# Kernel tuning notes

Measured on AMD Instinct MI355X. Metric: run time of the kernel, lower is better.

The kernel has to match this reference:

```python
import jax, jax.numpy as jnp
import numpy as np

D = 768        # d_model
F = 8192       # dict_size
N_UP = 3       # number of upstream autoencoders
K = 64         # topk
B, S = 2, 1024


def setup_inputs() -> dict:
    key = jax.random.key(0)
    ks = jax.random.split(key, 10)
    sc = 1.0 / np.sqrt(D)
    return {
        "feature_buffer": jnp.zeros((B, S, F), jnp.float32),
        "x": jax.random.normal(ks[0], (B, S, D), jnp.float32),
        "up_feats": jax.random.uniform(ks[1], (N_UP, B, S, F), jnp.float32),
        "W_enc": jax.random.normal(ks[2], (D, F), jnp.float32) * sc,
        "b_enc": jax.random.normal(ks[3], (F,), jnp.float32) * 0.01,
        "W_dec": jax.random.normal(ks[4], (F, D), jnp.float32) * sc,
        "b_dec": jax.random.normal(ks[5], (D,), jnp.float32) * 0.01,
        "up_W_dec": jax.random.normal(ks[6], (N_UP, F, D), jnp.float32) * sc,
        "up_b_dec": jax.random.normal(ks[7], (N_UP, D), jnp.float32) * 0.01,
        "conn_mask": jax.random.randint(ks[8], (N_UP, F, F), 0, 2).astype(bool),
        "k": K,
    }


def reference(feature_buffer, x, up_feats, W_enc, b_enc, W_dec, b_dec,
              up_W_dec, up_b_dec, conn_mask, k):
    # initial contribs: residual stream through current encoder
    approx = jnp.einsum("bsd,df->bsf", x, W_enc)            # [B,S,F]
    upstream_bias = jnp.zeros((D,), x.dtype)
    # accumulate pruned contributions from each upstream AE
    for i in range(up_feats.shape[0]):
        upstream_bias = upstream_bias + up_b_dec[i]
        # virtual weights up_dict -> down_dict, pruned by connection mask
        virt = (up_W_dec[i] @ W_enc) * conn_mask[i].astype(x.dtype)  # [F_up,F_down]
        approx = approx + jnp.einsum("bsf,fg->bsg", up_feats[i], virt)
    # bias correction: upstream decoder biases through encoder, plus encoder bias
    approx = approx + upstream_bias @ W_enc + b_enc          # [B,S,F]
    # topk + relu + scatter into the feature buffer
    top_vals, top_idx = jax.lax.top_k(approx, k)             # [B,S,k]
    top_vals = jax.nn.relu(top_vals)
    flat = feature_buffer.reshape(-1, F)
    rows = jnp.arange(flat.shape[0])[:, None]
    feat = flat.at[rows, top_idx.reshape(-1, k)].set(top_vals.reshape(-1, k))
    feat = feat.reshape(feature_buffer.shape)
    # decode
    return jnp.einsum("bsf,fd->bsd", feat, W_dec) + b_dec
```

## Files before the change

### kernel.cpp

```cpp
#include <hip/hip_runtime.h>
#include <hip/hip_bf16.h>


#define D_DIM 768
#define F_DIM 8192

typedef _Float16 f16;
typedef _Float16 f16x8 __attribute__((ext_vector_type(8)));
typedef float f32x4 __attribute__((ext_vector_type(4)));

#define BMN 128
#define BKK 64
#define LDSPLANE 16384

__device__ inline void split_f32(float v, f16& h, f16& l) {
    float hf = (float)(f16)v;
    if (__builtin_fabsf(hf) < 6.1035156e-5f) hf = 0.f;
    h = (f16)hf;
    l = (f16)((v - hf) * 2048.0f);
}

template<int MODE>
__global__ __launch_bounds__(256, 2)
void mfma_gemm(const f16* __restrict__ Ahp, const f16* __restrict__ Alp, int lda,
               const f16* __restrict__ Bhp, const f16* __restrict__ Blp, int ldb,
               float* __restrict__ C, int ldc,
               f16* __restrict__ Vh, f16* __restrict__ Vl,
               const float* __restrict__ bias,
               const unsigned char* __restrict__ conn, int upIdx,
               const int* __restrict__ flagp,
               int K, int fdBase)
{
    __shared__ char lds[65536];
    const int tid = threadIdx.x;
    const int bm = blockIdx.y * BMN;
    const int bn = blockIdx.x * BMN;
    const int w  = tid >> 6;
    const int l  = tid & 63;
    const int wr = (w >> 1) * 64;
    const int wc = (w & 1) * 64;

    const char* gsrc[16];
    #pragma unroll
    for (int j = 0; j < 16; ++j) {
        const int c = tid + 256 * j;
        const int p = c >> 10;
        const int q = c & 1023;
        const int r = q >> 3;
        const int sp = q & 7;
        const int slog = sp ^ (r & 7);
        const f16* base; int ld; int row0;
        if (p == 0)      { base = Ahp; ld = lda; row0 = bm; }
        else if (p == 1) { base = Alp; ld = lda; row0 = bm; }
        else if (p == 2) { base = Bhp; ld = ldb; row0 = bn; }
        else             { base = Blp; ld = ldb; row0 = bn; }
        gsrc[j] = (const char*)(base + (size_t)(row0 + r) * ld) + slog * 16;
    }

    f32x4 accH[4][4], accM[4][4];
    const f32x4 zero = {0.f, 0.f, 0.f, 0.f};
    #pragma unroll
    for (int a = 0; a < 4; ++a)
        #pragma unroll
        for (int b = 0; b < 4; ++b) { accH[a][b] = zero; accM[a][b] = zero; }

    const int steps = K >> 6;
    for (int t = 0; t < steps; ++t) {
        __syncthreads();
        #pragma unroll
        for (int j = 0; j < 16; ++j) {
            __builtin_amdgcn_global_load_lds(
                (const __attribute__((address_space(1))) void*)gsrc[j],
                (__attribute__((address_space(3))) void*)(lds + (tid + 256 * j) * 16),
                16, 0, 0);
            gsrc[j] += 128;
        }
        __syncthreads();

        #pragma unroll
        for (int kb = 0; kb < 2; ++kb) {
            const int slot = kb * 4 + (l >> 4);
            const int fr = l & 15;
            f16x8 ah[4], bh[4];
            #pragma unroll
            for (int mf = 0; mf < 4; ++mf) {
                const int r = wr + mf * 16 + fr;
                ah[mf] = *(const f16x8*)(lds + 0 * LDSPLANE + r * 128 + (slot ^ (r & 7)) * 16);
            }
            #pragma unroll
            for (int nf = 0; nf < 4; ++nf) {
                const int r = wc + nf * 16 + fr;
                bh[nf] = *(const f16x8*)(lds + 2 * LDSPLANE + r * 128 + (slot ^ (r & 7)) * 16);
            }
            #pragma unroll
            for (int nf = 0; nf < 4; ++nf)
                #pragma unroll
                for (int mf = 0; mf < 4; ++mf)
                    accH[mf][nf] = __builtin_amdgcn_mfma_f32_16x16x32_f16(
                        ah[mf], bh[nf], accH[mf][nf], 0, 0, 0);
            #pragma unroll
            for (int nf = 0; nf < 4; ++nf) {
                const int r = wc + nf * 16 + fr;
                const f16x8 bl = *(const f16x8*)(lds + 3 * LDSPLANE + r * 128 + (slot ^ (r & 7)) * 16);
                #pragma unroll
                for (int mf = 0; mf < 4; ++mf)
                    accM[mf][nf] = __builtin_amdgcn_mfma_f32_16x16x32_f16(
                        ah[mf], bl, accM[mf][nf], 0, 0, 0);
            }
            #pragma unroll
            for (int mf = 0; mf < 4; ++mf) {
                const int r = wr + mf * 16 + fr;
                const f16x8 al = *(const f16x8*)(lds + 1 * LDSPLANE + r * 128 + (slot ^ (r & 7)) * 16);
                #pragma unroll
                for (int nf = 0; nf < 4; ++nf)
                    accM[mf][nf] = __builtin_amdgcn_mfma_f32_16x16x32_f16(
                        al, bh[nf], accM[mf][nf], 0, 0, 0);
            }
        }
    }

    const float MS = 4.8828125e-4f;
    const int flag = (MODE == 1) ? *flagp : 0;

    #pragma unroll
    for (int mf = 0; mf < 4; ++mf) {
        const int row0 = wr + mf * 16 + (l >> 4) * 4;
        #pragma unroll
        for (int nf = 0; nf < 4; ++nf) {
            const int col = wc + nf * 16 + (l & 15);
            float v[4];
            #pragma unroll
            for (int rr = 0; rr < 4; ++rr)
                v[rr] = accH[mf][nf][rr] + accM[mf][nf][rr] * MS;

            if (MODE == 0) {
                const float bb = bias[bn + col];
                #pragma unroll
                for (int rr = 0; rr < 4; ++rr)
                    C[(size_t)(bm + row0 + rr) * ldc + (bn + col)] = v[rr] + bb;
            } else if (MODE == 2) {
                #pragma unroll
                for (int rr = 0; rr < 4; ++rr) {
                    float* cp = &C[(size_t)(bm + row0 + rr) * ldc + (bn + col)];
                    *cp = *cp + v[rr];
                }
            } else {
                const size_t fu = (size_t)(bn + col);
                const size_t fd0 = (size_t)(fdBase + bm + row0);
                int m[4];
                if (flag == 1) {
                    const int4 mm = *(const int4*)((const int*)conn +
                        (size_t)upIdx * F_DIM * F_DIM + fu * F_DIM + fd0);
                    m[0] = mm.x; m[1] = mm.y; m[2] = mm.z; m[3] = mm.w;
                } else if (flag == 0) {
                    const uchar4 mm = *(const uchar4*)(conn +
                        (size_t)upIdx * F_DIM * F_DIM + fu * F_DIM + fd0);
                    m[0] = mm.x; m[1] = mm.y; m[2] = mm.z; m[3] = mm.w;
                } else if (flag == 2) {
                    const long long* pp = (const long long*)conn +
                        (size_t)upIdx * F_DIM * F_DIM + fu * F_DIM + fd0;
                    m[0] = (int)pp[0]; m[1] = (int)pp[1];
                    m[2] = (int)pp[2]; m[3] = (int)pp[3];
                } else {
                    const float4 mm = *(const float4*)((const float*)conn +
                        (size_t)upIdx * F_DIM * F_DIM + fu * F_DIM + fd0);
                    m[0] = mm.x != 0.f; m[1] = mm.y != 0.f;
                    m[2] = mm.z != 0.f; m[3] = mm.w != 0.f;
                }
                #pragma unroll
                for (int rr = 0; rr < 4; ++rr) {
                    const float vv = m[rr] ? v[rr] : 0.f;
                    f16 hh, ll;
                    split_f32(vv, hh, ll);
                    const size_t o = (size_t)(bm + row0 + rr) * F_DIM + fu;
                    Vh[o] = hh; Vl[o] = ll;
                }
            }
        }
    }
}

__global__ __launch_bounds__(256)
void split_kernel(const float* __restrict__ src, f16* __restrict__ h,
                  f16* __restrict__ l, size_t n)
{
    const size_t e = ((size_t)blockIdx.x * 256 + threadIdx.x) * 8;
    if (e >= n) return;
    const float4 a = *(const float4*)(src + e);
    const float4 b = *(const float4*)(src + e + 4);
    f16 hv[8], lv[8];
    const float s[8] = {a.x, a.y, a.z, a.w, b.x, b.y, b.z, b.w};
    #pragma unroll
    for (int i = 0; i < 8; ++i) split_f32(s[i], hv[i], lv[i]);
    *(f16x8*)(h + e) = *(const f16x8*)hv;
    *(f16x8*)(l + e) = *(const f16x8*)lv;
}

__global__ __launch_bounds__(256)
void transpose_split_kernel(const float* __restrict__ W,
                            f16* __restrict__ th, f16* __restrict__ tl)
{
    const int f = blockIdx.x * 256 + threadIdx.x;
    for (int dc = 0; dc < D_DIM / 8; ++dc) {
        f16 hv[8], lv[8];
        #pragma unroll
        for (int j = 0; j < 8; ++j)
            split_f32(W[(size_t)(dc * 8 + j) * F_DIM + f], hv[j], lv[j]);
        *(f16x8*)(th + (size_t)f * D_DIM + dc * 8) = *(const f16x8*)hv;
        *(f16x8*)(tl + (size_t)f * D_DIM + dc * 8) = *(const f16x8*)lv;
    }
}

__global__ void detect_kernel(const int* __restrict__ conn, int* __restrict__ flag)
{
    __shared__ int not01, notf01, odd_nz;
    if (threadIdx.x == 0) { not01 = 0; notf01 = 0; odd_nz = 0; }
    __syncthreads();
    const int4 v = ((const int4*)conn)[threadIdx.x];
    const unsigned a[4] = {(unsigned)v.x, (unsigned)v.y,
                           (unsigned)v.z, (unsigned)v.w};
    int l_not01 = 0, l_notf = 0;
    #pragma unroll
    for (int i = 0; i < 4; ++i) {
        if (a[i] > 1u) l_not01 = 1;
        if (a[i] != 0u && a[i] != 0x3F800000u) l_notf = 1;
    }
    if (l_not01) atomicOr(&not01, 1);
    if (l_notf)  atomicOr(&notf01, 1);
    if (a[1] | a[3]) atomicOr(&odd_nz, 1);
    __syncthreads();
    if (threadIdx.x == 0) {
        int f;
        if (!not01)        f = odd_nz ? 1 : 2;
        else if (!notf01)  f = 3;
        else               f = 0;
        *flag = f;
    }
}

__global__ void bias2_kernel(const float* __restrict__ W_enc,
                             const float* __restrict__ b_enc,
                             const float* __restrict__ up_b_dec,
                             int nup, float* __restrict__ bias2)
{
    const int g = blockIdx.x * 256 + threadIdx.x;
    if (g >= F_DIM) return;
    float s = b_enc[g];
    for (int d = 0; d < D_DIM; ++d) {
        float ub = 0.f;
        for (int i = 0; i < nup; ++i) ub += up_b_dec[i * D_DIM + d];
        s = __builtin_fmaf(ub, W_enc[(size_t)d * F_DIM + g], s);
    }
    bias2[g] = s;
}

__global__ __launch_bounds__(256)
void topk_decode_kernel(const float* __restrict__ approx,
                        const float* __restrict__ W_dec,
                        const float* __restrict__ b_dec,
                        const int* __restrict__ kptr,
                        float* __restrict__ out)
{
    __shared__ unsigned keys[F_DIM];
    __shared__ int hist[256];
    __shared__ unsigned sh_prefix;
    __shared__ int sh_need;
    __shared__ int sel_cnt, eq_cnt;
    __shared__ int sidx[128];
    __shared__ float sval[128];
    __shared__ int eqidx[1024];

    const int tid = threadIdx.x;
    const int row = blockIdx.x;
    const int k = *kptr;
    const float* arow = approx + (size_t)row * F_DIM;

    for (int j = tid; j < F_DIM; j += 256) {
        unsigned u = __float_as_uint(arow[j]);
        u = (u & 0x80000000u) ? ~u : (u | 0x80000000u);
        keys[j] = u;
    }
    if (tid == 0) { sh_prefix = 0u; sh_need = k; sel_cnt = 0; eq_cnt = 0; }
    __syncthreads();

    for (int shift = 24; shift >= 0; shift -= 8) {
        if (tid < 256) hist[tid] = 0;
        __syncthreads();
        const unsigned pfx = sh_prefix;
        for (int j = tid; j < F_DIM; j += 256) {
            const unsigned u = keys[j];
            const bool match =
                (shift == 24) || ((u >> (shift + 8)) == (pfx >> (shift + 8)));
            if (match) atomicAdd(&hist[(u >> shift) & 255], 1);
        }
        __syncthreads();
        if (tid == 0) {
            int need = sh_need;
            for (int b = 255; b >= 0; --b) {
                const int c = hist[b];
                if (c >= need) {
                    sh_prefix = pfx | ((unsigned)b << shift);
                    sh_need = need;
                    break;
                }
                need -= c;
            }
        }
        __syncthreads();
    }
    const unsigned T = sh_prefix;
    const int r = sh_need;

    for (int j = tid; j < F_DIM; j += 256) {
        const unsigned u = keys[j];
        if (u > T) {
            const int p = atomicAdd(&sel_cnt, 1);
            sidx[p] = j;
        } else if (u == T) {
            const int p = atomicAdd(&eq_cnt, 1);
            if (p < 1024) eqidx[p] = j;
        }
    }
    __syncthreads();

    if (tid == 0) {
        const int m = sel_cnt;
        const int e = eq_cnt < 1024 ? eq_cnt : 1024;
        for (int t2 = 0; t2 < r; ++t2) {
            int best = 0x7FFFFFFF, bi = -1;
            for (int q = 0; q < e; ++q) {
                const int v = eqidx[q];
                if (v >= 0 && v < best) { best = v; bi = q; }
            }
            if (bi >= 0) { eqidx[bi] = -1; sidx[m + t2] = best; }
        }
        sel_cnt = m + r;
        const int n = sel_cnt;
        for (int a2 = 1; a2 < n; ++a2) {
            const int v = sidx[a2];
            int b2 = a2 - 1;
            while (b2 >= 0 && sidx[b2] > v) { sidx[b2 + 1] = sidx[b2]; --b2; }
            sidx[b2 + 1] = v;
        }
    }
    __syncthreads();

    const int total = sel_cnt;
    for (int j = tid; j < total; j += 256) {
        const float v = arow[sidx[j]];
        sval[j] = v > 0.f ? v : 0.f;
    }
    __syncthreads();

    float acc0 = b_dec[tid];
    float acc1 = b_dec[tid + 256];
    float acc2 = b_dec[tid + 512];
    for (int j = 0; j < total; ++j) {
        const float v = sval[j];
        const float* wv = W_dec + (size_t)sidx[j] * D_DIM;
        acc0 = __builtin_fmaf(v, wv[tid],       acc0);
        acc1 = __builtin_fmaf(v, wv[tid + 256], acc1);
        acc2 = __builtin_fmaf(v, wv[tid + 512], acc2);
    }
    float* orow = out + (size_t)row * D_DIM;
    orow[tid] = acc0;
    orow[tid + 256] = acc1;
    orow[tid + 512] = acc2;
}

extern "C" void kernel_launch(void* const* d_in, const int* in_sizes, int n_in,
                              void* d_out, int out_size, void* d_ws, size_t ws_size,
                              hipStream_t stream)
{
    const float* x         = (const float*)d_in[1];
    const float* up_feats  = (const float*)d_in[2];
    const float* W_enc     = (const float*)d_in[3];
    const float* b_enc     = (const float*)d_in[4];
    const float* W_dec     = (const float*)d_in[5];
    const float* b_dec     = (const float*)d_in[6];
    const float* up_W_dec  = (const float*)d_in[7];
    const float* up_b_dec  = (const float*)d_in[8];
    const unsigned char* conn = (const unsigned char*)d_in[9];
    const int* kptr        = (const int*)d_in[10];

    const int BS  = in_sizes[1] / D_DIM;
    const int NUP = in_sizes[8] / D_DIM;

    char* ws = (char*)d_ws;
    size_t off = 0;
    auto alloc = [&](size_t bytes) -> char* {
        off = (off + 255) & ~(size_t)255;
        char* p = ws + off; off += bytes; return p;
    };
    float* approx = (float*)alloc((size_t)BS * F_DIM * 4);
    float* bias2  = (float*)alloc(F_DIM * 4);
    int*   flag   = (int*)alloc(256);
    f16* xh  = (f16*)alloc((size_t)BS * D_DIM * 2);
    f16* xl  = (f16*)alloc((size_t)BS * D_DIM * 2);
    f16* Wth = (f16*)alloc((size_t)F_DIM * D_DIM * 2);
    f16* Wtl = (f16*)alloc((size_t)F_DIM * D_DIM * 2);
    f16* uwdh = (f16*)alloc((size_t)NUP * F_DIM * D_DIM * 2);
    f16* uwdl = (f16*)alloc((size_t)NUP * F_DIM * D_DIM * 2);
    f16* ufh = (f16*)alloc((size_t)NUP * BS * F_DIM * 2);
    f16* ufl = (f16*)alloc((size_t)NUP * BS * F_DIM * 2);

    off = (off + 255) & ~(size_t)255;
    const size_t rem = (ws_size > off) ? ws_size - off : 0;
    int FC = (int)((rem / ((size_t)F_DIM * 2 * 2)) / 128 * 128);
    if (FC > F_DIM) FC = F_DIM;
    if (FC < 128) FC = 128;
    f16* vh = (f16*)alloc((size_t)FC * F_DIM * 2);
    f16* vl = (f16*)alloc((size_t)FC * F_DIM * 2);

    detect_kernel<<<1, 256, 0, stream>>>((const int*)conn, flag);
    bias2_kernel<<<F_DIM / 256, 256, 0, stream>>>(W_enc, b_enc, up_b_dec, NUP, bias2);

    split_kernel<<<(unsigned)((size_t)BS * D_DIM / 2048), 256, 0, stream>>>(
        x, xh, xl, (size_t)BS * D_DIM);
    split_kernel<<<(unsigned)((size_t)NUP * F_DIM * D_DIM / 2048), 256, 0, stream>>>(
        up_W_dec, uwdh, uwdl, (size_t)NUP * F_DIM * D_DIM);
    split_kernel<<<(unsigned)((size_t)NUP * BS * F_DIM / 2048), 256, 0, stream>>>(
        up_feats, ufh, ufl, (size_t)NUP * BS * F_DIM);
    transpose_split_kernel<<<F_DIM / 256, 256, 0, stream>>>(W_enc, Wth, Wtl);

    mfma_gemm<0><<<dim3(F_DIM / BMN, BS / BMN), 256, 0, stream>>>(
        xh, xl, D_DIM, Wth, Wtl, D_DIM,
        approx, F_DIM, nullptr, nullptr, bias2,
        nullptr, 0, flag, D_DIM, 0);

    for (int i = 0; i < NUP; ++i) {
        for (int fc = 0; fc < F_DIM; fc += FC) {
            const int chunk = (F_DIM - fc) < FC ? (F_DIM - fc) : FC;
            mfma_gemm<1><<<dim3(F_DIM / BMN, chunk / BMN), 256, 0, stream>>>(
                Wth + (size_t)fc * D_DIM, Wtl + (size_t)fc * D_DIM, D_DIM,
                uwdh + (size_t)i * F_DIM * D_DIM, uwdl + (size_t)i * F_DIM * D_DIM, D_DIM,
                nullptr, 0, vh, vl, nullptr,
                conn, i, flag, D_DIM, fc);
            mfma_gemm<2><<<dim3(chunk / BMN, BS / BMN), 256, 0, stream>>>(
                ufh + (size_t)i * BS * F_DIM, ufl + (size_t)i * BS * F_DIM, F_DIM,
                vh, vl, F_DIM,
                approx + fc, F_DIM, nullptr, nullptr, nullptr,
                nullptr, 0, flag, F_DIM, 0);
        }
    }

    topk_decode_kernel<<<BS, 256, 0, stream>>>(
        approx, W_dec, b_dec, kptr, (float*)d_out);
}
```

Before: 3.977 ms.

## Double-buffer LDS tiles with K=32 stages to overlap global loads with MFMA

Shrinks each K-step from 64 to 32 and packs the hi and lo f16 planes of each operand into one interleaved 128-byte row. This lets two 32KB buffers fit in the same 64KB of LDS. The next stage's global_load_lds is issued right after the barrier, so loads overlap the MFMAs on the current buffer. The barriers per unit of K double, and each iteration waits on vmcnt(0), which limits how much overlap it can actually get.

```diff
diff --git a/kernel.cpp b/kernel.cpp
--- a/kernel.cpp
+++ b/kernel.cpp
@@ -10,8 +10,8 @@
 typedef float f32x4 __attribute__((ext_vector_type(4)));
 
 #define BMN 128
-#define BKK 64
-#define LDSPLANE 16384
+#define BUFB 32768
+#define PLNB 16384
 
 __device__ inline void split_f32(float v, f16& h, f16& l) {
     float hf = (float)(f16)v;
@@ -31,7 +31,7 @@
                const int* __restrict__ flagp,
                int K, int fdBase)
 {
-    __shared__ char lds[65536];
+    __shared__ char lds[2 * BUFB];
     const int tid = threadIdx.x;
     const int bm = blockIdx.y * BMN;
     const int bn = blockIdx.x * BMN;
@@ -40,22 +40,33 @@
     const int wr = (w >> 1) * 64;
     const int wc = (w & 1) * 64;
 
-    const char* gsrc[16];
+    const char* gsrc[8];
     #pragma unroll
-    for (int j = 0; j < 16; ++j) {
+    for (int j = 0; j < 8; ++j) {
         const int c = tid + 256 * j;
         const int p = c >> 10;
         const int q = c & 1023;
         const int r = q >> 3;
         const int sp = q & 7;
         const int slog = sp ^ (r & 7);
-        const f16* base; int ld; int row0;
-        if (p == 0)      { base = Ahp; ld = lda; row0 = bm; }
-        else if (p == 1) { base = Alp; ld = lda; row0 = bm; }
-        else if (p == 2) { base = Bhp; ld = ldb; row0 = bn; }
-        else             { base = Blp; ld = ldb; row0 = bn; }
-        gsrc[j] = (const char*)(base + (size_t)(row0 + r) * ld) + slog * 16;
-    }
+        const f16* hb = p ? Bhp : Ahp;
+        const f16* lb = p ? Blp : Alp;
+        const int ld  = p ? ldb : lda;
+        const int row0 = p ? bn : bm;
+        const f16* base = (slog < 4) ? hb : lb;
+        gsrc[j] = (const char*)(base + (size_t)(row0 + r) * ld + (slog & 3) * 8);
+    }
+
+    #define STAGE(BUFSEL)                                                     \
+        _Pragma("unroll")                                                     \
+        for (int j = 0; j < 8; ++j) {                                         \
+            __builtin_amdgcn_global_load_lds(                                 \
+                (const __attribute__((address_space(1))) void*)gsrc[j],       \
+                (__attribute__((address_space(3))) void*)                     \
+                    (lds + (BUFSEL) * BUFB + (tid + 256 * j) * 16),           \
+                16, 0, 0);                                                    \
+            gsrc[j] += 64;                        \
+        }
 
     f32x4 accH[4][4], accM[4][4];
     const f32x4 zero = {0.f, 0.f, 0.f, 0.f};
@@ -64,60 +75,58 @@
         #pragma unroll
         for (int b = 0; b < 4; ++b) { accH[a][b] = zero; accM[a][b] = zero; }
 
-    const int steps = K >> 6;
+    const int steps = K >> 5;
+    const int fr = l & 15;
+    const int ks = l >> 4;
+
+    STAGE(0);
+    int cur = 0;
     for (int t = 0; t < steps; ++t) {
+        asm volatile("s_waitcnt vmcnt(0)" ::: "memory");
         __syncthreads();
-        #pragma unroll
-        for (int j = 0; j < 16; ++j) {
-            __builtin_amdgcn_global_load_lds(
-                (const __attribute__((address_space(1))) void*)gsrc[j],
-                (__attribute__((address_space(3))) void*)(lds + (tid + 256 * j) * 16),
-                16, 0, 0);
-            gsrc[j] += 128;
-        }
-        __syncthreads();
-
-        #pragma unroll
-        for (int kb = 0; kb < 2; ++kb) {
-            const int slot = kb * 4 + (l >> 4);
-            const int fr = l & 15;
-            f16x8 ah[4], bh[4];
+        if (t + 1 < steps) STAGE(cur ^ 1);
+
+        const char* Lb = lds + cur * BUFB;
+        f16x8 ah[4], bh[4];
+        #pragma unroll
+        for (int mf = 0; mf < 4; ++mf) {
+            const int r = wr + mf * 16 + fr;
+            ah[mf] = *(const f16x8*)(Lb + r * 128 + ((ks ^ (r & 7)) * 16));
+        }
+        #pragma unroll
+        for (int nf = 0; nf < 4; ++nf) {
+            const int r = wc + nf * 16 + fr;
+            bh[nf] = *(const f16x8*)(Lb + PLNB + r * 128 + ((ks ^ (r & 7)) * 16));
+        }
+        #pragma unroll
+        for (int nf = 0; nf < 4; ++nf)
             #pragma unroll
-            for (int mf = 0; mf < 4; ++mf) {
-                const int r = wr + mf * 16 + fr;
-                ah[mf] = *(const f16x8*)(lds + 0 * LDSPLANE + r * 128 + (slot ^ (r & 7)) * 16);
-            }
+            for (int mf = 0; mf < 4; ++mf)
+                accH[mf][nf] = __builtin_amdgcn_mfma_f32_16x16x32_f16(
+                    ah[mf], bh[nf], accH[mf][nf], 0, 0, 0);
+        #pragma unroll
+        for (int nf = 0; nf < 4; ++nf) {
+            const int r = wc + nf * 16 + fr;
+            const f16x8 bl = *(const f16x8*)(Lb + PLNB + r * 128 +
+                                             (((4 + ks) ^ (r & 7)) * 16));
             #pragma unroll
-            for (int nf = 0; nf < 4; ++nf) {
-                const int r = wc + nf * 16 + fr;
-                bh[nf] = *(const f16x8*)(lds + 2 * LDSPLANE + r * 128 + (slot ^ (r & 7)) * 16);
-            }
+            for (int mf = 0; mf < 4; ++mf)
+                accM[mf][nf] = __builtin_amdgcn_mfma_f32_16x16x32_f16(
+                    ah[mf], bl, accM[mf][nf], 0, 0, 0);
+        }
+        #pragma unroll
+        for (int mf = 0; mf < 4; ++mf) {
+            const int r = wr + mf * 16 + fr;
+            const f16x8 al = *(const f16x8*)(Lb + r * 128 +
+                                             (((4 + ks) ^ (r & 7)) * 16));
             #pragma unroll
             for (int nf = 0; nf < 4; ++nf)
-                #pragma unroll
-                for (int mf = 0; mf < 4; ++mf)
-                    accH[mf][nf] = __builtin_amdgcn_mfma_f32_16x16x32_f16(
-                        ah[mf], bh[nf], accH[mf][nf], 0, 0, 0);
-            #pragma unroll
-            for (int nf = 0; nf < 4; ++nf) {
-                const int r = wc + nf * 16 + fr;
-                const f16x8 bl = *(const f16x8*)(lds + 3 * LDSPLANE + r * 128 + (slot ^ (r & 7)) * 16);
-                #pragma unroll
-                for (int mf = 0; mf < 4; ++mf)
-                    accM[mf][nf] = __builtin_amdgcn_mfma_f32_16x16x32_f16(
-                        ah[mf], bl, accM[mf][nf], 0, 0, 0);
-            }
-            #pragma unroll
-            for (int mf = 0; mf < 4; ++mf) {
-                const int r = wr + mf * 16 + fr;
-                const f16x8 al = *(const f16x8*)(lds + 1 * LDSPLANE + r * 128 + (slot ^ (r & 7)) * 16);
-                #pragma unroll
-                for (int nf = 0; nf < 4; ++nf)
-                    accM[mf][nf] = __builtin_amdgcn_mfma_f32_16x16x32_f16(
-                        al, bh[nf], accM[mf][nf], 0, 0, 0);
-            }
-        }
-    }
+                accM[mf][nf] = __builtin_amdgcn_mfma_f32_16x16x32_f16(
+                    al, bh[nf], accM[mf][nf], 0, 0, 0);
+        }
+        cur ^= 1;
+    }
+    #undef STAGE
 
     const float MS = 4.8828125e-4f;
     const int flag = (MODE == 1) ? *flagp : 0;
```

New measurement: 4.363 ms. 9.7% more time.
